# Optimization experiments

Hardware: AMD Instinct MI355X
Metric: run time of the kernel (lower is better)

The kernel has to match this reference:

```python
import jax, jax.numpy as jnp
import numpy as np

N_NODES = 50000
N_EDGES = 800000
IN_CH = 128
OUT_CH = 64
HEADS = 4
NEG_SLOPE = 0.2  # PyG GATConv default


def setup_inputs() -> dict:
    key = jax.random.key(0)
    k1, k2, k3, k4, k5 = jax.random.split(key, 5)
    x = jax.random.normal(k1, (N_NODES, IN_CH), dtype=jnp.float32)
    edge_index = jax.random.randint(k2, (2, N_EDGES), 0, N_NODES, dtype=jnp.int64)
    W = jax.random.normal(k3, (HEADS * OUT_CH, IN_CH), dtype=jnp.float32) * (1.0 / np.sqrt(IN_CH))
    att_src = jax.random.normal(k4, (HEADS, OUT_CH), dtype=jnp.float32) * (1.0 / np.sqrt(OUT_CH))
    att_dst = jax.random.normal(k5, (HEADS, OUT_CH), dtype=jnp.float32) * (1.0 / np.sqrt(OUT_CH))
    bias = jnp.zeros((OUT_CH,), dtype=jnp.float32)
    return {"x": x, "edge_index": edge_index, "W": W,
            "att_src": att_src, "att_dst": att_dst, "bias": bias}


def reference(x, edge_index, W, att_src, att_dst, bias):
    # GAT2NO_NORM.forward in eval mode: dropout == identity.
    N = x.shape[0]
    H, C = att_src.shape
    # PyG GATConv adds self-loops by default.
    loop = jnp.arange(N, dtype=edge_index.dtype)
    src = jnp.concatenate([edge_index[0], loop])  # message source j
    dst = jnp.concatenate([edge_index[1], loop])  # message target i
    # Linear projection, reshape to heads: [N, H, C]
    h = (x @ W.T).reshape(N, H, C)
    # Per-node attention halves: [N, H]
    a_src = jnp.einsum('nhc,hc->nh', h, att_src)
    a_dst = jnp.einsum('nhc,hc->nh', h, att_dst)
    # Per-edge raw score, LeakyReLU: [E, H]
    e = jax.nn.leaky_relu(a_src[src] + a_dst[dst], NEG_SLOPE)
    # Segment (edge-)softmax over incoming edges of each dst node.
    m = jax.lax.stop_gradient(jax.ops.segment_max(e, dst, num_segments=N))
    ex = jnp.exp(e - m[dst])
    denom = jax.ops.segment_sum(ex, dst, num_segments=N)
    alpha = ex / denom[dst]  # self-loops guarantee denom > 0
    # Weighted scatter-sum of messages: [N, H, C]
    msg = h[src] * alpha[:, :, None]
    out = jax.ops.segment_sum(msg, dst, num_segments=N)
    # concat=False -> mean over heads, then bias, then ReLU (module wrapper)
    out = out.mean(axis=1) + bias
    return jax.nn.relu(out)
```

## Files before the change

### kernel.cpp

```cpp
#include <hip/hip_runtime.h>
#include <hip/hip_fp16.h>
#include <math.h>

#define N_NODES 50000
#define N_EDGES 800000
#define IN_CH 128
#define PROJ_CH 256
#define OUT_CH 64
#define HEADS 4
#define NEG_SLOPE 0.2f
#define NREP 8
#define CAP8 20
#define CAPT (NREP * CAP8)
#define SLOTS 192
#define MEGA_BLOCKS 782
#define EPB 1024

typedef _Float16 f16x8 __attribute__((ext_vector_type(8)));
typedef _Float16 f16x4 __attribute__((ext_vector_type(4)));
typedef __fp16   hf2   __attribute__((ext_vector_type(2)));
typedef float    f32x4 __attribute__((ext_vector_type(4)));

__device__ __forceinline__ float leaky(float v) {
    return v > 0.f ? v : NEG_SLOPE * v;
}

__device__ __forceinline__ hf2 u32_as_h2(unsigned int u) {
    union { unsigned int u; hf2 h; } c; c.u = u; return c.h;
}

__global__ __launch_bounds__(256) void prep_kernel(
    const float* __restrict__ W, _Float16* __restrict__ Wh, int* __restrict__ cnt8)
{
    const int t = blockIdx.x * 256 + threadIdx.x;
    if (t < PROJ_CH * IN_CH) Wh[t] = (_Float16)W[t];
    if (t < NREP * N_NODES) cnt8[t] = 0;
}

__global__ __launch_bounds__(256) void mega_kernel(
    const float* __restrict__ x, const _Float16* __restrict__ Wh,
    const float* __restrict__ att_src, const float* __restrict__ att_dst,
    const int* __restrict__ ei, int* __restrict__ cnt8, unsigned short* __restrict__ csr8,
    _Float16* __restrict__ h, float* __restrict__ a_src, float* __restrict__ a_dst)
{
    __shared__ _Float16 xs[64 * 136];
    const int tid = threadIdx.x;
    const int bid = blockIdx.x;
    const int rep = bid & (NREP - 1);

    const int e0 = bid * EPB + tid;
    int es[4], ed[4], pos[4];
#pragma unroll
    for (int r = 0; r < 4; ++r) {
        const int e = e0 + r * 256;
        const bool v = e < N_EDGES;
        es[r] = v ? ei[e] : 0;
        ed[r] = v ? ei[N_EDGES + e] : 0;
        pos[r] = CAP8;
        if (v) pos[r] = atomicAdd(&cnt8[rep * N_NODES + ed[r]], 1);
    }

    const int w    = tid >> 6;
    const int lane = tid & 63;
    const int q    = lane >> 4;
    const int l15  = lane & 15;
    const int nb   = bid * 64;

    f16x8 B[4][4];
#pragma unroll
    for (int k0i = 0; k0i < 4; ++k0i)
#pragma unroll
        for (int n0i = 0; n0i < 4; ++n0i) {
            const int oc = w * 64 + n0i * 16 + l15;
            B[k0i][n0i] = *(const f16x8*)(Wh + (size_t)oc * IN_CH + k0i * 32 + q * 8);
        }

#pragma unroll
    for (int r = 0; r < 8; ++r) {
        int v   = r * 256 + tid;
        int row = v >> 5;
        int c4  = v & 31;
        int grow = nb + row;
        if (grow > N_NODES - 1) grow = N_NODES - 1;
        float4 xv = *(const float4*)(x + (size_t)grow * IN_CH + c4 * 4);
        f16x4 hv;
        hv[0] = (_Float16)xv.x; hv[1] = (_Float16)xv.y;
        hv[2] = (_Float16)xv.z; hv[3] = (_Float16)xv.w;
        *(f16x4*)&xs[row * 136 + c4 * 4] = hv;
    }
    __syncthreads();

    f32x4 acc[4][4];
#pragma unroll
    for (int m0i = 0; m0i < 4; ++m0i)
#pragma unroll
        for (int n0i = 0; n0i < 4; ++n0i)
            acc[m0i][n0i] = (f32x4){0.f, 0.f, 0.f, 0.f};

#pragma unroll
    for (int k0i = 0; k0i < 4; ++k0i) {
        f16x8 A[4];
#pragma unroll
        for (int m0i = 0; m0i < 4; ++m0i)
            A[m0i] = *(const f16x8*)&xs[(m0i * 16 + l15) * 136 + k0i * 32 + q * 8];
#pragma unroll
        for (int n0i = 0; n0i < 4; ++n0i)
#pragma unroll
            for (int m0i = 0; m0i < 4; ++m0i)
                acc[m0i][n0i] = __builtin_amdgcn_mfma_f32_16x16x32_f16(
                    A[m0i], B[k0i][n0i], acc[m0i][n0i], 0, 0, 0);
    }

    float att_s[4], att_d[4];
#pragma unroll
    for (int n0i = 0; n0i < 4; ++n0i) {
        att_s[n0i] = att_src[w * 64 + n0i * 16 + l15];
        att_d[n0i] = att_dst[w * 64 + n0i * 16 + l15];
    }

#pragma unroll
    for (int m0i = 0; m0i < 4; ++m0i) {
        float vs[4], vd[4];
#pragma unroll
        for (int r = 0; r < 4; ++r) {
            float s = 0.f, d = 0.f;
#pragma unroll
            for (int n0i = 0; n0i < 4; ++n0i) {
                s = fmaf(acc[m0i][n0i][r], att_s[n0i], s);
                d = fmaf(acc[m0i][n0i][r], att_d[n0i], d);
            }
            vs[r] = s; vd[r] = d;
        }
#pragma unroll
        for (int off = 1; off < 16; off <<= 1) {
#pragma unroll
            for (int r = 0; r < 4; ++r) {
                vs[r] += __shfl_xor(vs[r], off, 64);
                vd[r] += __shfl_xor(vd[r], off, 64);
            }
        }
#pragma unroll
        for (int r = 0; r < 4; ++r) {
            int node = nb + m0i * 16 + q * 4 + r;
            if (l15 == 0 && node < N_NODES) {
                a_src[node * HEADS + w] = vs[r];
                a_dst[node * HEADS + w] = vd[r];
            }
        }
#pragma unroll
        for (int r = 0; r < 4; ++r) {
            int node = nb + m0i * 16 + q * 4 + r;
            if (node < N_NODES) {
#pragma unroll
                for (int n0i = 0; n0i < 4; ++n0i)
                    h[(size_t)node * PROJ_CH + w * 64 + n0i * 16 + l15] =
                        (_Float16)acc[m0i][n0i][r];
            }
        }
    }

#pragma unroll
    for (int r = 0; r < 4; ++r)
        if (pos[r] < CAP8)
            csr8[((size_t)rep * N_NODES + ed[r]) * CAP8 + pos[r]] = (unsigned short)es[r];
}

__global__ __launch_bounds__(256) void aggregate_kernel(
    const _Float16* __restrict__ h, const float* __restrict__ a_src,
    const float* __restrict__ a_dst, const int* __restrict__ cnt8,
    const unsigned short* __restrict__ csr8, const float* __restrict__ bias,
    float* __restrict__ out)
{
    const int tid  = threadIdx.x;
    const int wave = tid >> 6;
    const int l    = tid & 63;
    const int i    = blockIdx.x * 4 + wave;

    __shared__ float lw_all[4][HEADS * SLOTS];
    __shared__ int   lj_all[4][SLOTS];
    float* lw = lw_all[wave];
    int*   lj = lj_all[wave];

    const int gr = l >> 3;
    const int gk = l & 7;
    int nr_g = 0, base_g = 0, m = 0;
#pragma unroll
    for (int r = 0; r < NREP; ++r) {
        int c = cnt8[r * N_NODES + i];
        c = min(c, CAP8);
        if (r == gr) { nr_g = c; base_g = m; }
        m += c;
    }
    if (l == 0) lj[0] = i << 9;
    {
        const size_t cbase = ((size_t)gr * N_NODES + i) * CAP8;
#pragma unroll
        for (int kk = 0; kk < CAP8; kk += 8) {
            int k = gk + kk;
            if (k < nr_g) lj[1 + base_g + k] = ((int)csr8[cbase + k]) << 9;
        }
    }

    const int h4   = l & 3;
    const float adh = a_dst[i * 4 + h4];
    const char* ab = (const char*)a_src;

    float lsum = 0.f;
    {
        float ws = __expf(leaky(a_src[i * 4 + h4] + adh));
        if (l < 4) { lw[l * SLOTS] = ws; lsum = ws; }
    }

    const int T  = m + 1;
    const int Tp = (T + 15) & ~15;
    const int erel = l >> 2;
    for (int s0 = 0; s0 < Tp - 1; s0 += 16) {
        const int e = s0 + erel;
        const bool valid = e < m;
        float w = 0.f;
        if (valid) {
            int sj = lj[e + 1];
            w = __expf(leaky(*(const float*)(ab + (sj >> 5) + h4 * 4) + adh));
        } else if (h4 == 0) {
            lj[e + 1] = 0;
        }
        lsum += w;
        lw[h4 * SLOTS + e + 1] = w;
    }
#pragma unroll
    for (int off = 4; off < 64; off <<= 1) lsum += __shfl_xor(lsum, off, 64);

    __syncthreads();

    const int half_ = l >> 5;
    const int jj    = l & 31;
    const int hd    = jj >> 3;
    const unsigned jjb = (unsigned)jj * 16u;
    const char* hb = (const char*)h;
    const float* lwh = lw + hd * SLOTS;

    float acc[8];
#pragma unroll
    for (int k = 0; k < 8; ++k) acc[k] = 0.f;

    for (int qq = 0; qq < Tp; qq += 16) {
        const int eb = qq + 8 * half_;
        int o[8];
#pragma unroll
        for (int k = 0; k < 8; ++k) o[k] = lj[eb + k];
        uint4 d[8];
#pragma unroll
        for (int k = 0; k < 8; ++k)
            d[k] = *(const uint4*)(hb + ((unsigned)o[k] + jjb));

        hf2 wp[4];
#pragma unroll
        for (int pr = 0; pr < 4; ++pr) {
            float2 wf = *(const float2*)&lwh[eb + 2 * pr];
            wp[pr] = __builtin_amdgcn_cvt_pkrtz(wf.x, wf.y);
        }

#pragma unroll
        for (int pr = 0; pr < 4; ++pr) {
            const unsigned int* Aa = (const unsigned int*)&d[2 * pr];
            const unsigned int* Ab = (const unsigned int*)&d[2 * pr + 1];
#pragma unroll
            for (int k = 0; k < 4; ++k) {
                unsigned int lo = __builtin_amdgcn_perm(Ab[k], Aa[k], 0x05040100u);
                unsigned int hi = __builtin_amdgcn_perm(Ab[k], Aa[k], 0x07060302u);
                acc[2 * k]     = __builtin_amdgcn_fdot2(u32_as_h2(lo), wp[pr], acc[2 * k], false);
                acc[2 * k + 1] = __builtin_amdgcn_fdot2(u32_as_h2(hi), wp[pr], acc[2 * k + 1], false);
            }
        }
    }

#pragma unroll
    for (int k = 0; k < 8; ++k) acc[k] += __shfl_xor(acc[k], 32, 64);

    float linv = 1.f / __shfl(lsum, hd, 64);
#pragma unroll
    for (int k = 0; k < 8; ++k) {
        float r = acc[k] * linv;
        r += __shfl_xor(r, 8, 64);
        r += __shfl_xor(r, 16, 64);
        acc[k] = r;
    }

    if (l < 8) {
        float* op = out + (size_t)i * OUT_CH + l * 8;
        float4 o0, o1;
        o0.x = fmaxf(0.25f * acc[0] + bias[l * 8 + 0], 0.f);
        o0.y = fmaxf(0.25f * acc[1] + bias[l * 8 + 1], 0.f);
        o0.z = fmaxf(0.25f * acc[2] + bias[l * 8 + 2], 0.f);
        o0.w = fmaxf(0.25f * acc[3] + bias[l * 8 + 3], 0.f);
        o1.x = fmaxf(0.25f * acc[4] + bias[l * 8 + 4], 0.f);
        o1.y = fmaxf(0.25f * acc[5] + bias[l * 8 + 5], 0.f);
        o1.z = fmaxf(0.25f * acc[6] + bias[l * 8 + 6], 0.f);
        o1.w = fmaxf(0.25f * acc[7] + bias[l * 8 + 7], 0.f);
        *(float4*)op = o0;
        *((float4*)op + 1) = o1;
    }
}

extern "C" void kernel_launch(void* const* d_in, const int* in_sizes, int n_in,
                              void* d_out, int out_size, void* d_ws, size_t ws_size,
                              hipStream_t stream)
{
    const float* x       = (const float*)d_in[0];
    const int*   ei      = (const int*)d_in[1];
    const float* W       = (const float*)d_in[2];
    const float* att_src = (const float*)d_in[3];
    const float* att_dst = (const float*)d_in[4];
    const float* bias    = (const float*)d_in[5];
    float* out = (float*)d_out;

    _Float16* h  = (_Float16*)d_ws;
    float* asrc  = (float*)(h + (size_t)N_NODES * PROJ_CH);
    float* adst  = asrc + (size_t)N_NODES * HEADS;
    int*   cnt8  = (int*)(adst + (size_t)N_NODES * HEADS);
    unsigned short* csr8 = (unsigned short*)(cnt8 + NREP * N_NODES);
    _Float16* Wh = (_Float16*)(csr8 + (size_t)NREP * N_NODES * CAP8);

    hipLaunchKernelGGL(prep_kernel, dim3((NREP * N_NODES + 255) / 256), dim3(256), 0, stream,
                       W, Wh, cnt8);
    hipLaunchKernelGGL(mega_kernel, dim3(MEGA_BLOCKS), dim3(256), 0, stream,
                       x, Wh, att_src, att_dst, ei, cnt8, csr8, h, asrc, adst);
    hipLaunchKernelGGL(aggregate_kernel, dim3(N_NODES / 4), dim3(256), 0, stream,
                       h, asrc, adst, cnt8, csr8, bias, out);
}
```

Baseline: 201.0 us.

## Split edge scatter from projection, reorder loads, and halve aggregation edge batch

The fused projection+CSR-scatter kernel is split into a standalone scatter kernel with one edge per thread and a projection-only kernel. In the projection kernel, x loads are issued before the weight loads to overlap memory latency. The aggregation loop now gathers 4 edges per half-wave instead of 8, padding the edge count to 8 rather than 16, which cuts wasted gathers on low-degree nodes. The price is an extra kernel launch and fewer loads in flight per iteration.

```diff
diff --git a/kernel.cpp b/kernel.cpp
--- a/kernel.cpp
+++ b/kernel.cpp
@@ -12,9 +12,9 @@
 #define NREP 8
 #define CAP8 20
 #define CAPT (NREP * CAP8)
-#define SLOTS 192
-#define MEGA_BLOCKS 782
-#define EPB 1024
+#define SLOTS 208
+#define PROJ_BLOCKS 782
+#define SCAT_BLOCKS 3125
 
 typedef _Float16 f16x8 __attribute__((ext_vector_type(8)));
 typedef _Float16 f16x4 __attribute__((ext_vector_type(4)));
@@ -37,28 +37,25 @@
     if (t < NREP * N_NODES) cnt8[t] = 0;
 }
 
-__global__ __launch_bounds__(256) void mega_kernel(
+__global__ __launch_bounds__(256) void scatter_kernel(
+    const int* __restrict__ ei, int* __restrict__ cnt8, unsigned short* __restrict__ csr8)
+{
+    const int e = blockIdx.x * 256 + threadIdx.x;
+    const int rep = blockIdx.x & (NREP - 1);
+    const int esrc = ei[e];
+    const int edst = ei[N_EDGES + e];
+    const int pos = atomicAdd(&cnt8[rep * N_NODES + edst], 1);
+    if (pos < CAP8) csr8[((size_t)rep * N_NODES + edst) * CAP8 + pos] = (unsigned short)esrc;
+}
+
+__global__ __launch_bounds__(256) void proj_kernel(
     const float* __restrict__ x, const _Float16* __restrict__ Wh,
     const float* __restrict__ att_src, const float* __restrict__ att_dst,
-    const int* __restrict__ ei, int* __restrict__ cnt8, unsigned short* __restrict__ csr8,
     _Float16* __restrict__ h, float* __restrict__ a_src, float* __restrict__ a_dst)
 {
     __shared__ _Float16 xs[64 * 136];
     const int tid = threadIdx.x;
     const int bid = blockIdx.x;
-    const int rep = bid & (NREP - 1);
-
-    const int e0 = bid * EPB + tid;
-    int es[4], ed[4], pos[4];
-#pragma unroll
-    for (int r = 0; r < 4; ++r) {
-        const int e = e0 + r * 256;
-        const bool v = e < N_EDGES;
-        es[r] = v ? ei[e] : 0;
-        ed[r] = v ? ei[N_EDGES + e] : 0;
-        pos[r] = CAP8;
-        if (v) pos[r] = atomicAdd(&cnt8[rep * N_NODES + ed[r]], 1);
-    }
 
     const int w    = tid >> 6;
     const int lane = tid & 63;
@@ -66,15 +63,7 @@
     const int l15  = lane & 15;
     const int nb   = bid * 64;
 
-    f16x8 B[4][4];
-#pragma unroll
-    for (int k0i = 0; k0i < 4; ++k0i)
-#pragma unroll
-        for (int n0i = 0; n0i < 4; ++n0i) {
-            const int oc = w * 64 + n0i * 16 + l15;
-            B[k0i][n0i] = *(const f16x8*)(Wh + (size_t)oc * IN_CH + k0i * 32 + q * 8);
-        }
-
+    float4 xv[8];
 #pragma unroll
     for (int r = 0; r < 8; ++r) {
         int v   = r * 256 + tid;
@@ -82,10 +71,26 @@
         int c4  = v & 31;
         int grow = nb + row;
         if (grow > N_NODES - 1) grow = N_NODES - 1;
-        float4 xv = *(const float4*)(x + (size_t)grow * IN_CH + c4 * 4);
+        xv[r] = *(const float4*)(x + (size_t)grow * IN_CH + c4 * 4);
+    }
+
+    f16x8 B[4][4];
+#pragma unroll
+    for (int k0i = 0; k0i < 4; ++k0i)
+#pragma unroll
+        for (int n0i = 0; n0i < 4; ++n0i) {
+            const int oc = w * 64 + n0i * 16 + l15;
+            B[k0i][n0i] = *(const f16x8*)(Wh + (size_t)oc * IN_CH + k0i * 32 + q * 8);
+        }
+
+#pragma unroll
+    for (int r = 0; r < 8; ++r) {
+        int v   = r * 256 + tid;
+        int row = v >> 5;
+        int c4  = v & 31;
         f16x4 hv;
-        hv[0] = (_Float16)xv.x; hv[1] = (_Float16)xv.y;
-        hv[2] = (_Float16)xv.z; hv[3] = (_Float16)xv.w;
+        hv[0] = (_Float16)xv[r].x; hv[1] = (_Float16)xv[r].y;
+        hv[2] = (_Float16)xv[r].z; hv[3] = (_Float16)xv[r].w;
         *(f16x4*)&xs[row * 136 + c4 * 4] = hv;
     }
     __syncthreads();
@@ -158,11 +163,6 @@
             }
         }
     }
-
-#pragma unroll
-    for (int r = 0; r < 4; ++r)
-        if (pos[r] < CAP8)
-            csr8[((size_t)rep * N_NODES + ed[r]) * CAP8 + pos[r]] = (unsigned short)es[r];
 }
 
 __global__ __launch_bounds__(256) void aggregate_kernel(
@@ -212,7 +212,7 @@
     }
 
     const int T  = m + 1;
-    const int Tp = (T + 15) & ~15;
+    const int Tp = (T + 7) & ~7;
     const int erel = l >> 2;
     for (int s0 = 0; s0 < Tp - 1; s0 += 16) {
         const int e = s0 + erel;
@@ -243,25 +243,25 @@
 #pragma unroll
     for (int k = 0; k < 8; ++k) acc[k] = 0.f;
 
-    for (int qq = 0; qq < Tp; qq += 16) {
-        const int eb = qq + 8 * half_;
-        int o[8];
-#pragma unroll
-        for (int k = 0; k < 8; ++k) o[k] = lj[eb + k];
-        uint4 d[8];
-#pragma unroll
-        for (int k = 0; k < 8; ++k)
+    for (int qq = 0; qq < Tp; qq += 8) {
+        const int eb = qq + 4 * half_;
+        int o[4];
+#pragma unroll
+        for (int k = 0; k < 4; ++k) o[k] = lj[eb + k];
+        uint4 d[4];
+#pragma unroll
+        for (int k = 0; k < 4; ++k)
             d[k] = *(const uint4*)(hb + ((unsigned)o[k] + jjb));
 
-        hf2 wp[4];
-#pragma unroll
-        for (int pr = 0; pr < 4; ++pr) {
+        hf2 wp[2];
+#pragma unroll
+        for (int pr = 0; pr < 2; ++pr) {
             float2 wf = *(const float2*)&lwh[eb + 2 * pr];
             wp[pr] = __builtin_amdgcn_cvt_pkrtz(wf.x, wf.y);
         }
 
 #pragma unroll
-        for (int pr = 0; pr < 4; ++pr) {
+        for (int pr = 0; pr < 2; ++pr) {
             const unsigned int* Aa = (const unsigned int*)&d[2 * pr];
             const unsigned int* Ab = (const unsigned int*)&d[2 * pr + 1];
 #pragma unroll
@@ -323,8 +323,10 @@
 
     hipLaunchKernelGGL(prep_kernel, dim3((NREP * N_NODES + 255) / 256), dim3(256), 0, stream,
                        W, Wh, cnt8);
-    hipLaunchKernelGGL(mega_kernel, dim3(MEGA_BLOCKS), dim3(256), 0, stream,
-                       x, Wh, att_src, att_dst, ei, cnt8, csr8, h, asrc, adst);
+    hipLaunchKernelGGL(scatter_kernel, dim3(SCAT_BLOCKS), dim3(256), 0, stream,
+                       ei, cnt8, csr8);
+    hipLaunchKernelGGL(proj_kernel, dim3(PROJ_BLOCKS), dim3(256), 0, stream,
+                       x, Wh, att_src, att_dst, h, asrc, adst);
     hipLaunchKernelGGL(aggregate_kernel, dim3(N_NODES / 4), dim3(256), 0, stream,
                        h, asrc, adst, cnt8, csr8, bias, out);
 }
```

Result: no change. 201.4 us (+0.2%).
